# Kernel tuning notes

Measured on AMD Instinct MI355X. Metric: run time of the kernel, lower is better.

## Reference

```python
import jax, jax.numpy as jnp
import numpy as np

B, L, D, A = 64, 512, 512, 512  # batch, seq_len, word_embed_size, alignment_size


def setup_inputs() -> dict:
    key = jax.random.key(0)
    k1, k2, k3 = jax.random.split(key, 3)
    premises = jax.random.normal(k1, (B, L, D), dtype=jnp.float32)
    hypotheses = jax.random.normal(k2, (B, L, D), dtype=jnp.float32)
    W_F = jax.random.uniform(k3, (D, A), dtype=jnp.float32, minval=-1.0, maxval=1.0)
    return {"premises": premises, "hypotheses": hypotheses, "W_F": W_F}


def reference(premises, hypotheses, W_F):
    # tanh-projected cross attention (decomposable-attention align step)
    F_p = jnp.tanh(jnp.einsum('bpd,da->bpa', premises, W_F))    # [B, Lp, A]
    F_h = jnp.tanh(jnp.einsum('bhd,da->bha', hypotheses, W_F))  # [B, Lh, A]
    eijs = jnp.einsum('bpa,bha->bph', F_p, F_h)                 # [B, Lp, Lh] (unscaled)
    attn = jax.nn.softmax(eijs, axis=-1)                        # softmax over hypothesis axis
    betas = jnp.einsum('bph,bhd->bpd', attn, hypotheses)        # [B, Lp, D]
    alphas = jnp.einsum('bph,bpd->bhd', attn, premises)         # [B, Lh, D] (transpose(attn) @ P)
    return betas, alphas
```

## Files before the change

kernel.cpp:

```cpp
#include <hip/hip_runtime.h>
#include <hip/hip_fp16.h>


#define NB 64
#define NL 512
#define ND 512
#define BATCH_ELEMS (512 * 512)
#define TOT_ELEMS   ((size_t)NB * NL * ND)

typedef _Float16 h8 __attribute__((ext_vector_type(8)));
typedef float f4 __attribute__((ext_vector_type(4)));

__device__ __forceinline__ int swz(int row, int chunk) {
    return (row << 5) + ((chunk ^ (((row >> 1) ^ (row >> 4)) & 3)) << 3);
}

__device__ __forceinline__ float fast_tanh(float x) {
    float e = __expf(2.0f * x);
    return 1.0f - 2.0f / (e + 1.0f);
}

template <bool WITH_LO>
__global__ __launch_bounds__(256) void transpose_f16_kernel(
    const float* __restrict__ src, _Float16* __restrict__ dstH,
    _Float16* __restrict__ dstL)
{
    __shared__ float tile[64 * 68];
    const size_t base = (size_t)blockIdx.z * BATCH_ELEMS;
    const int r0 = blockIdx.y * 64, c0 = blockIdx.x * 64;
    const int t = threadIdx.x;
    {
        int r = t >> 2, cq = (t & 3) * 16;
        const float* sp = src + base + (size_t)(r0 + r) * 512 + c0 + cq;
        *(float4*)&tile[r * 68 + cq]      = ((const float4*)sp)[0];
        *(float4*)&tile[r * 68 + cq + 4]  = ((const float4*)sp)[1];
        *(float4*)&tile[r * 68 + cq + 8]  = ((const float4*)sp)[2];
        *(float4*)&tile[r * 68 + cq + 12] = ((const float4*)sp)[3];
    }
    __syncthreads();
    {
        int c = t >> 2, rq = (t & 3) * 16;
        _Float16 hv[16], lv[16];
#pragma unroll
        for (int j = 0; j < 16; ++j) {
            float v = tile[(rq + j) * 68 + c];
            hv[j] = (_Float16)v;
            if (WITH_LO) lv[j] = (_Float16)(v - (float)hv[j]);
        }
        _Float16* dp = dstH + base + (size_t)(c0 + c) * 512 + r0 + rq;
        *(h8*)dp = *(h8*)&hv[0];
        *(h8*)(dp + 8) = *(h8*)&hv[8];
        if (WITH_LO) {
            _Float16* dl = dstL + base + (size_t)(c0 + c) * 512 + r0 + rq;
            *(h8*)dl = *(h8*)&lv[0];
            *(h8*)(dl + 8) = *(h8*)&lv[8];
        }
    }
}

__global__ __launch_bounds__(256) void proj_tanh_kernel(
    const float* __restrict__ P, const float* __restrict__ H,
    const _Float16* __restrict__ WTH, const _Float16* __restrict__ WTL,
    _Float16* __restrict__ Fout)
{
    __shared__ __align__(16) _Float16 AsH[128 * 32], AsL[128 * 32];
    __shared__ __align__(16) _Float16 BsH[128 * 32], BsL[128 * 32];

    const int z = blockIdx.z;
    const float* X = z ? H : P;
    _Float16* F = Fout + (size_t)z * TOT_ELEMS;
    const int r0 = blockIdx.x * 128;
    const int n0 = blockIdx.y * 128;

    const int t = threadIdx.x;
    const int lane = t & 63, w = t >> 6;
    const int q = lane >> 4, c = lane & 15;
    const int wm = w >> 1, wn = w & 1;

    f4 acc[4][4] = {};

    const int ar = t >> 1, akq = (t & 1) << 4;
    const int br = t >> 1, bcp = (t & 1) << 1;

    for (int k0 = 0; k0 < 512; k0 += 32) {
        {
            const float* ap = X + (size_t)(r0 + ar) * 512 + k0 + akq;
            float av[16];
            *(float4*)&av[0]  = ((const float4*)ap)[0];
            *(float4*)&av[4]  = ((const float4*)ap)[1];
            *(float4*)&av[8]  = ((const float4*)ap)[2];
            *(float4*)&av[12] = ((const float4*)ap)[3];
            const int cbase = akq >> 3;
#pragma unroll
            for (int jj = 0; jj < 2; ++jj) {
                h8 hv, lv;
#pragma unroll
                for (int i = 0; i < 8; ++i) {
                    float x = av[jj * 8 + i];
                    _Float16 hx = (_Float16)x;
                    hv[i] = hx;
                    lv[i] = (_Float16)(x - (float)hx);
                }
                *(h8*)&AsH[swz(ar, cbase + jj)] = hv;
                *(h8*)&AsL[swz(ar, cbase + jj)] = lv;
            }
        }
        {
            const _Float16* bh = WTH + (size_t)(n0 + br) * 512 + k0 + bcp * 8;
            const _Float16* bl = WTL + (size_t)(n0 + br) * 512 + k0 + bcp * 8;
            *(h8*)&BsH[swz(br, bcp)]     = ((const h8*)bh)[0];
            *(h8*)&BsH[swz(br, bcp + 1)] = ((const h8*)bh)[1];
            *(h8*)&BsL[swz(br, bcp)]     = ((const h8*)bl)[0];
            *(h8*)&BsL[swz(br, bcp + 1)] = ((const h8*)bl)[1];
        }
        __syncthreads();

        h8 aH[4], aL[4], bH[4], bL[4];
#pragma unroll
        for (int mi = 0; mi < 4; ++mi) {
            int row = wm * 64 + mi * 16 + c;
            aH[mi] = *(const h8*)&AsH[swz(row, q)];
            aL[mi] = *(const h8*)&AsL[swz(row, q)];
        }
#pragma unroll
        for (int ni = 0; ni < 4; ++ni) {
            int col = wn * 64 + ni * 16 + c;
            bH[ni] = *(const h8*)&BsH[swz(col, q)];
            bL[ni] = *(const h8*)&BsL[swz(col, q)];
        }
#pragma unroll
        for (int mi = 0; mi < 4; ++mi)
#pragma unroll
            for (int ni = 0; ni < 4; ++ni) {
                acc[mi][ni] = __builtin_amdgcn_mfma_f32_16x16x32_f16(aH[mi], bH[ni], acc[mi][ni], 0, 0, 0);
                acc[mi][ni] = __builtin_amdgcn_mfma_f32_16x16x32_f16(aH[mi], bL[ni], acc[mi][ni], 0, 0, 0);
                acc[mi][ni] = __builtin_amdgcn_mfma_f32_16x16x32_f16(aL[mi], bH[ni], acc[mi][ni], 0, 0, 0);
            }
        __syncthreads();
    }

#pragma unroll
    for (int mi = 0; mi < 4; ++mi)
#pragma unroll
        for (int ni = 0; ni < 4; ++ni) {
            int col = n0 + wn * 64 + ni * 16 + c;
            int rowb = r0 + wm * 64 + mi * 16 + q * 4;
#pragma unroll
            for (int r = 0; r < 4; ++r)
                F[(size_t)(rowb + r) * 512 + col] = (_Float16)fast_tanh(acc[mi][ni][r]);
        }
}

__global__ __launch_bounds__(256) void score_softmax_kernel(
    const _Float16* __restrict__ Fbase, _Float16* __restrict__ attn)
{
    __shared__ __align__(16) _Float16 As[64 * 32];
    __shared__ __align__(16) _Float16 Bs[512 * 32];
    __shared__ float redM[4 * 64], redS[4 * 64];

    const _Float16* Fp = Fbase;
    const _Float16* Fh = Fbase + TOT_ELEMS;
    const int b = blockIdx.y;
    const int p0 = blockIdx.x * 64;
    const size_t fb = (size_t)b * BATCH_ELEMS;

    const int t = threadIdx.x, lane = t & 63, w = t >> 6;
    const int q = lane >> 4, c = lane & 15;

    f4 acc[4][8] = {};

    for (int k0 = 0; k0 < 512; k0 += 32) {
        {
            int row = t >> 2, ch = t & 3;
            *(h8*)&As[swz(row, ch)] =
                *(const h8*)(Fp + fb + (size_t)(p0 + row) * 512 + k0 + ch * 8);
        }
        {
#pragma unroll
            for (int rr = 0; rr < 2; ++rr) {
                int row = t * 2 + rr;
#pragma unroll
                for (int ch = 0; ch < 4; ++ch)
                    *(h8*)&Bs[swz(row, ch)] =
                        *(const h8*)(Fh + fb + (size_t)row * 512 + k0 + ch * 8);
            }
        }
        __syncthreads();

        h8 a[4], bb[8];
#pragma unroll
        for (int mt = 0; mt < 4; ++mt) a[mt] = *(const h8*)&As[swz(mt * 16 + c, q)];
#pragma unroll
        for (int nt = 0; nt < 8; ++nt) bb[nt] = *(const h8*)&Bs[swz(w * 128 + nt * 16 + c, q)];
#pragma unroll
        for (int mt = 0; mt < 4; ++mt)
#pragma unroll
            for (int nt = 0; nt < 8; ++nt)
                acc[mt][nt] = __builtin_amdgcn_mfma_f32_16x16x32_f16(a[mt], bb[nt], acc[mt][nt], 0, 0, 0);
        __syncthreads();
    }

    float rmax[4][4];
#pragma unroll
    for (int mt = 0; mt < 4; ++mt)
#pragma unroll
        for (int r = 0; r < 4; ++r) {
            float m = acc[mt][0][r];
#pragma unroll
            for (int nt = 1; nt < 8; ++nt) m = fmaxf(m, acc[mt][nt][r]);
            rmax[mt][r] = m;
        }
#pragma unroll
    for (int s = 1; s < 16; s <<= 1)
#pragma unroll
        for (int mt = 0; mt < 4; ++mt)
#pragma unroll
            for (int r = 0; r < 4; ++r)
                rmax[mt][r] = fmaxf(rmax[mt][r], __shfl_xor(rmax[mt][r], s, 64));
    if (c == 0)
#pragma unroll
        for (int mt = 0; mt < 4; ++mt)
#pragma unroll
            for (int r = 0; r < 4; ++r)
                redM[w * 64 + mt * 16 + q * 4 + r] = rmax[mt][r];
    __syncthreads();

    float gmax[4][4];
#pragma unroll
    for (int mt = 0; mt < 4; ++mt)
#pragma unroll
        for (int r = 0; r < 4; ++r) {
            int row = mt * 16 + q * 4 + r;
            float m = redM[row];
#pragma unroll
            for (int w4 = 1; w4 < 4; ++w4) m = fmaxf(m, redM[w4 * 64 + row]);
            gmax[mt][r] = m;
        }

    float rsum[4][4] = {};
#pragma unroll
    for (int mt = 0; mt < 4; ++mt)
#pragma unroll
        for (int nt = 0; nt < 8; ++nt)
#pragma unroll
            for (int r = 0; r < 4; ++r) {
                float e = __expf(acc[mt][nt][r] - gmax[mt][r]);
                acc[mt][nt][r] = e;
                rsum[mt][r] += e;
            }
#pragma unroll
    for (int s = 1; s < 16; s <<= 1)
#pragma unroll
        for (int mt = 0; mt < 4; ++mt)
#pragma unroll
            for (int r = 0; r < 4; ++r)
                rsum[mt][r] += __shfl_xor(rsum[mt][r], s, 64);
    if (c == 0)
#pragma unroll
        for (int mt = 0; mt < 4; ++mt)
#pragma unroll
            for (int r = 0; r < 4; ++r)
                redS[w * 64 + mt * 16 + q * 4 + r] = rsum[mt][r];
    __syncthreads();

    float inv[4][4];
#pragma unroll
    for (int mt = 0; mt < 4; ++mt)
#pragma unroll
        for (int r = 0; r < 4; ++r) {
            int row = mt * 16 + q * 4 + r;
            float s = redS[row] + redS[64 + row] + redS[128 + row] + redS[192 + row];
            inv[mt][r] = 1.0f / s;
        }

#pragma unroll
    for (int mt = 0; mt < 4; ++mt)
#pragma unroll
        for (int nt = 0; nt < 8; ++nt) {
            int col = w * 128 + nt * 16 + c;
#pragma unroll
            for (int r = 0; r < 4; ++r) {
                int row = p0 + mt * 16 + q * 4 + r;
                attn[fb + (size_t)row * 512 + col] = (_Float16)(acc[mt][nt][r] * inv[mt][r]);
            }
        }
}

template <bool TRANS_A>
__global__ __launch_bounds__(256) void out_gemm_kernel(
    const _Float16* __restrict__ Amat, const _Float16* __restrict__ BT,
    float* __restrict__ Cout)
{
    __shared__ __align__(16) _Float16 As[128 * 32];
    __shared__ __align__(16) _Float16 Bs[128 * 32];

    const int b = blockIdx.z;
    const int bn = blockIdx.x * 128, bm = blockIdx.y * 128;
    const size_t base = (size_t)b * BATCH_ELEMS;

    const int t = threadIdx.x, lane = t & 63, w = t >> 6;
    const int q = lane >> 4, c = lane & 15;
    const int wm = w >> 1, wn = w & 1;

    f4 acc[4][4] = {};

    for (int k0 = 0; k0 < 512; k0 += 32) {
        if (!TRANS_A) {
            int row = t >> 1, cp = (t & 1) * 2;
            const _Float16* ap = Amat + base + (size_t)(bm + row) * 512 + k0 + cp * 8;
            *(h8*)&As[swz(row, cp)]     = ((const h8*)ap)[0];
            *(h8*)&As[swz(row, cp + 1)] = ((const h8*)ap)[1];
        } else {
            int kk = t >> 3, m0 = (t & 7) * 16;
            const _Float16* ap = Amat + base + (size_t)(k0 + kk) * 512 + bm + m0;
            h8 x0 = ((const h8*)ap)[0];
            h8 x1 = ((const h8*)ap)[1];
#pragma unroll
            for (int j = 0; j < 8; ++j) {
                As[swz(m0 + j, kk >> 3) + (kk & 7)]     = x0[j];
                As[swz(m0 + 8 + j, kk >> 3) + (kk & 7)] = x1[j];
            }
        }
        {
            int row = t >> 1, cp = (t & 1) * 2;
            const _Float16* bp = BT + base + (size_t)(bn + row) * 512 + k0 + cp * 8;
            *(h8*)&Bs[swz(row, cp)]     = ((const h8*)bp)[0];
            *(h8*)&Bs[swz(row, cp + 1)] = ((const h8*)bp)[1];
        }
        __syncthreads();

        h8 a[4], bb[4];
#pragma unroll
        for (int mi = 0; mi < 4; ++mi) a[mi] = *(const h8*)&As[swz(wm * 64 + mi * 16 + c, q)];
#pragma unroll
        for (int ni = 0; ni < 4; ++ni) bb[ni] = *(const h8*)&Bs[swz(wn * 64 + ni * 16 + c, q)];
#pragma unroll
        for (int mi = 0; mi < 4; ++mi)
#pragma unroll
            for (int ni = 0; ni < 4; ++ni)
                acc[mi][ni] = __builtin_amdgcn_mfma_f32_16x16x32_f16(a[mi], bb[ni], acc[mi][ni], 0, 0, 0);
        __syncthreads();
    }

#pragma unroll
    for (int mi = 0; mi < 4; ++mi)
#pragma unroll
        for (int ni = 0; ni < 4; ++ni) {
            int col = bn + wn * 64 + ni * 16 + c;
            int rowb = bm + wm * 64 + mi * 16 + q * 4;
#pragma unroll
            for (int r = 0; r < 4; ++r)
                Cout[base + (size_t)(rowb + r) * 512 + col] = acc[mi][ni][r];
        }
}

extern "C" void kernel_launch(void* const* d_in, const int* in_sizes, int n_in,
                              void* d_out, int out_size, void* d_ws, size_t ws_size,
                              hipStream_t stream) {
    const float* P = (const float*)d_in[0];
    const float* H = (const float*)d_in[1];
    const float* W = (const float*)d_in[2];
    float* out = (float*)d_out;

    _Float16* ws16 = (_Float16*)d_ws;
    _Float16* F    = ws16;
    _Float16* PT   = ws16;
    _Float16* HT   = ws16 + TOT_ELEMS;
    _Float16* attn = ws16 + 2 * TOT_ELEMS;
    _Float16* WTH  = attn;
    _Float16* WTL  = attn + BATCH_ELEMS;

    transpose_f16_kernel<true><<<dim3(8, 8, 1), 256, 0, stream>>>(W, WTH, WTL);
    proj_tanh_kernel<<<dim3(256, 4, 2), 256, 0, stream>>>(P, H, WTH, WTL, F);
    score_softmax_kernel<<<dim3(8, NB), 256, 0, stream>>>(F, attn);
    transpose_f16_kernel<false><<<dim3(8, 8, NB), 256, 0, stream>>>(H, HT, nullptr);
    transpose_f16_kernel<false><<<dim3(8, 8, NB), 256, 0, stream>>>(P, PT, nullptr);
    out_gemm_kernel<false><<<dim3(4, 4, NB), 256, 0, stream>>>(attn, HT, out);
    out_gemm_kernel<true><<<dim3(4, 4, NB), 256, 0, stream>>>(attn, PT, out + TOT_ELEMS);
}
```

Baseline: 502.7 us.

## Drop activation low-part split in projection and merge transpose and output GEMM launches

```diff
diff --git a/kernel.cpp b/kernel.cpp
--- a/kernel.cpp
+++ b/kernel.cpp
@@ -58,12 +58,43 @@
     }
 }
 
+__global__ __launch_bounds__(256) void transpose_hp_kernel(
+    const float* __restrict__ H, const float* __restrict__ P,
+    _Float16* __restrict__ HT, _Float16* __restrict__ PT)
+{
+    __shared__ float tile[64 * 68];
+    const int z = blockIdx.z;
+    const float* src = (z < NB) ? H : P;
+    _Float16* dst = (z < NB) ? HT : PT;
+    const size_t base = (size_t)(z < NB ? z : z - NB) * BATCH_ELEMS;
+    const int r0 = blockIdx.y * 64, c0 = blockIdx.x * 64;
+    const int t = threadIdx.x;
+    {
+        int r = t >> 2, cq = (t & 3) * 16;
+        const float* sp = src + base + (size_t)(r0 + r) * 512 + c0 + cq;
+        *(float4*)&tile[r * 68 + cq]      = ((const float4*)sp)[0];
+        *(float4*)&tile[r * 68 + cq + 4]  = ((const float4*)sp)[1];
+        *(float4*)&tile[r * 68 + cq + 8]  = ((const float4*)sp)[2];
+        *(float4*)&tile[r * 68 + cq + 12] = ((const float4*)sp)[3];
+    }
+    __syncthreads();
+    {
+        int c = t >> 2, rq = (t & 3) * 16;
+        _Float16 hv[16];
+#pragma unroll
+        for (int j = 0; j < 16; ++j) hv[j] = (_Float16)tile[(rq + j) * 68 + c];
+        _Float16* dp = dst + base + (size_t)(c0 + c) * 512 + r0 + rq;
+        *(h8*)dp = *(h8*)&hv[0];
+        *(h8*)(dp + 8) = *(h8*)&hv[8];
+    }
+}
+
 __global__ __launch_bounds__(256) void proj_tanh_kernel(
     const float* __restrict__ P, const float* __restrict__ H,
     const _Float16* __restrict__ WTH, const _Float16* __restrict__ WTL,
     _Float16* __restrict__ Fout)
 {
-    __shared__ __align__(16) _Float16 AsH[128 * 32], AsL[128 * 32];
+    __shared__ __align__(16) _Float16 AsH[128 * 32];
     __shared__ __align__(16) _Float16 BsH[128 * 32], BsL[128 * 32];
 
     const int z = blockIdx.z;
@@ -93,16 +124,10 @@
             const int cbase = akq >> 3;
 #pragma unroll
             for (int jj = 0; jj < 2; ++jj) {
-                h8 hv, lv;
-#pragma unroll
-                for (int i = 0; i < 8; ++i) {
-                    float x = av[jj * 8 + i];
-                    _Float16 hx = (_Float16)x;
-                    hv[i] = hx;
-                    lv[i] = (_Float16)(x - (float)hx);
-                }
+                h8 hv;
+#pragma unroll
+                for (int i = 0; i < 8; ++i) hv[i] = (_Float16)av[jj * 8 + i];
                 *(h8*)&AsH[swz(ar, cbase + jj)] = hv;
-                *(h8*)&AsL[swz(ar, cbase + jj)] = lv;
             }
         }
         {
@@ -115,12 +140,11 @@
         }
         __syncthreads();
 
-        h8 aH[4], aL[4], bH[4], bL[4];
+        h8 aH[4], bH[4], bL[4];
 #pragma unroll
         for (int mi = 0; mi < 4; ++mi) {
             int row = wm * 64 + mi * 16 + c;
             aH[mi] = *(const h8*)&AsH[swz(row, q)];
-            aL[mi] = *(const h8*)&AsL[swz(row, q)];
         }
 #pragma unroll
         for (int ni = 0; ni < 4; ++ni) {
@@ -134,7 +158,6 @@
             for (int ni = 0; ni < 4; ++ni) {
                 acc[mi][ni] = __builtin_amdgcn_mfma_f32_16x16x32_f16(aH[mi], bH[ni], acc[mi][ni], 0, 0, 0);
                 acc[mi][ni] = __builtin_amdgcn_mfma_f32_16x16x32_f16(aH[mi], bL[ni], acc[mi][ni], 0, 0, 0);
-                acc[mi][ni] = __builtin_amdgcn_mfma_f32_16x16x32_f16(aL[mi], bH[ni], acc[mi][ni], 0, 0, 0);
             }
         __syncthreads();
     }
@@ -286,15 +309,19 @@
         }
 }
 
-template <bool TRANS_A>
 __global__ __launch_bounds__(256) void out_gemm_kernel(
-    const _Float16* __restrict__ Amat, const _Float16* __restrict__ BT,
-    float* __restrict__ Cout)
+    const _Float16* __restrict__ Amat, const _Float16* __restrict__ HT,
+    const _Float16* __restrict__ PT, float* __restrict__ out)
 {
     __shared__ __align__(16) _Float16 As[128 * 32];
     __shared__ __align__(16) _Float16 Bs[128 * 32];
 
-    const int b = blockIdx.z;
+    const int zz = blockIdx.z;
+    const bool transA = zz >= NB;
+    const int b = transA ? zz - NB : zz;
+    const _Float16* BT = transA ? PT : HT;
+    float* Cout = transA ? out + TOT_ELEMS : out;
+
     const int bn = blockIdx.x * 128, bm = blockIdx.y * 128;
     const size_t base = (size_t)b * BATCH_ELEMS;
 
@@ -305,7 +332,7 @@
     f4 acc[4][4] = {};
 
     for (int k0 = 0; k0 < 512; k0 += 32) {
-        if (!TRANS_A) {
+        if (!transA) {
             int row = t >> 1, cp = (t & 1) * 2;
             const _Float16* ap = Amat + base + (size_t)(bm + row) * 512 + k0 + cp * 8;
             *(h8*)&As[swz(row, cp)]     = ((const h8*)ap)[0];
@@ -373,8 +400,6 @@
     transpose_f16_kernel<true><<<dim3(8, 8, 1), 256, 0, stream>>>(W, WTH, WTL);
     proj_tanh_kernel<<<dim3(256, 4, 2), 256, 0, stream>>>(P, H, WTH, WTL, F);
     score_softmax_kernel<<<dim3(8, NB), 256, 0, stream>>>(F, attn);
-    transpose_f16_kernel<false><<<dim3(8, 8, NB), 256, 0, stream>>>(H, HT, nullptr);
-    transpose_f16_kernel<false><<<dim3(8, 8, NB), 256, 0, stream>>>(P, PT, nullptr);
-    out_gemm_kernel<false><<<dim3(4, 4, NB), 256, 0, stream>>>(attn, HT, out);
-    out_gemm_kernel<true><<<dim3(4, 4, NB), 256, 0, stream>>>(attn, PT, out + TOT_ELEMS);
-}
+    transpose_hp_kernel<<<dim3(8, 8, 2 * NB), 256, 0, stream>>>(H, P, HT, PT);
+    out_gemm_kernel<<<dim3(4, 4, 2 * NB), 256, 0, stream>>>(attn, HT, PT, out);
+}
```

Result: faster. 481.2 us (-4.3%).
